# Kernel tuning notes

Hardware: AMD Instinct MI355X
Metric: run time of the kernel (lower is better)

The kernel has to match this reference:

```python
import jax, jax.numpy as jnp
import numpy as np

N, D = 4096, 2048

def setup_inputs() -> dict:
    key = jax.random.key(0)
    k1, k2 = jax.random.split(key)
    Ws = jax.random.normal(k1, (N, D), dtype=jnp.float32)
    # nn.Bilinear(D, D, 1): weight [1, D, D], bias [1]
    W = jax.random.normal(k2, (1, D, D), dtype=jnp.float32) * (1.0 / np.sqrt(D))
    b = jnp.zeros((1,), dtype=jnp.float32)
    return {"Ws": Ws, "W": W, "b": b}

def reference(Ws, W, b):
    # A[i, j] = Ws[i] @ W[0] @ Ws[j] + b[0]  (bilinear score for every pair)
    t = Ws @ W[0]                 # [N, D]
    A = t @ Ws.T + b[0]           # [N, N]
    return jax.nn.softmax(A, axis=1)
```

## Files before the change

### kernel.cpp

```cpp
#include <hip/hip_runtime.h>

typedef __bf16 bf16x8 __attribute__((ext_vector_type(8)));
typedef float f32x4 __attribute__((ext_vector_type(4)));
typedef unsigned short u16;
typedef u16 u16x8 __attribute__((ext_vector_type(8)));

#define AS1 __attribute__((address_space(1)))
#define AS3 __attribute__((address_space(3)))

__device__ __forceinline__ void split2(float x, u16& h, u16& l) {
  __bf16 hb = (__bf16)x;
  float hf = (float)hb;
  __bf16 lb = (__bf16)(x - hf);
  h = __builtin_bit_cast(u16, hb);
  l = __builtin_bit_cast(u16, lb);
}

__global__ __launch_bounds__(256) void k_pack_ws(const float* __restrict__ X,
                                                 u16* __restrict__ P) {
  const int total8 = (4096 * 2048) / 8;
  for (int idx = blockIdx.x * 256 + threadIdx.x; idx < total8; idx += gridDim.x * 256) {
    int row = idx >> 8;
    int k8  = idx & 255;
    const float* src = X + ((size_t)row << 11) + (k8 << 3);
    const float4 v0 = *(const float4*)src;
    const float4 v1 = *(const float4*)(src + 4);
    float xv[8] = {v0.x, v0.y, v0.z, v0.w, v1.x, v1.y, v1.z, v1.w};
    u16x8 hv, lv;
#pragma unroll
    for (int j = 0; j < 8; ++j) { u16 h, l; split2(xv[j], h, l); hv[j] = h; lv[j] = l; }
    size_t base = ((size_t)row << 12) + (size_t)((k8 >> 2) << 6) + ((k8 & 3) << 3);
    *(u16x8*)(P + base) = hv;
    *(u16x8*)(P + base + 32) = lv;
  }
}

__global__ __launch_bounds__(256) void k_transpose_pack_w(const float* __restrict__ W,
                                                          u16* __restrict__ P) {
  __shared__ float tile[32][33];
  const int tx = threadIdx.x, ty = threadIdx.y;
  const int kbase = blockIdx.y << 5, cbase = blockIdx.x << 5;
#pragma unroll
  for (int i = 0; i < 4; ++i)
    tile[ty * 4 + i][tx] = W[((size_t)(kbase + ty * 4 + i) << 11) + cbase + tx];
  __syncthreads();
#pragma unroll
  for (int i = 0; i < 4; ++i) {
    int c = cbase + ty * 4 + i;
    float v = tile[tx][ty * 4 + i];
    u16 h, l; split2(v, h, l);
    size_t base = ((size_t)c << 12) + (size_t)(kbase << 1) + tx;
    P[base] = h;
    P[base + 32] = l;
  }
}

template <bool SPLIT_OUT>
__global__ __launch_bounds__(256, 2) void k_gemm_nt(const u16* __restrict__ Ap,
                                                    const u16* __restrict__ Bp,
                                                    float* __restrict__ Cout,
                                                    u16* __restrict__ Cpack,
                                                    const int Ncols) {
  __shared__ __align__(16) u16 lds_a[128 * 64];
  __shared__ __align__(16) u16 lds_b[128 * 64];
  const int tid = threadIdx.x;
  const int lane = tid & 63, w = tid >> 6;
  const int wr = w >> 1, wc = w & 1;
  const int row0 = blockIdx.y << 7, col0 = blockIdx.x << 7;
  const int lrow = lane & 15, kg = lane >> 4;

  f32x4 acc[4][4] = {};

  const u16* abase = Ap + ((size_t)row0 << 12);
  const u16* bbase = Bp + ((size_t)col0 << 12);

  int offAh[4], offAl[4], offBh[4], offBl[4];
#pragma unroll
  for (int m = 0; m < 4; ++m) {
    int r = wr * 64 + m * 16 + lrow;
    int sw = r & 7;
    offAh[m] = r * 64 + ((kg ^ sw) << 3);
    offAl[m] = r * 64 + (((4 + kg) ^ sw) << 3);
    int rb = wc * 64 + m * 16 + lrow;
    int swb = rb & 7;
    offBh[m] = rb * 64 + ((kg ^ swb) << 3);
    offBl[m] = rb * 64 + (((4 + kg) ^ swb) << 3);
  }

  for (int kb = 0; kb < 64; ++kb) {
    const int kofs = kb << 6;
#pragma unroll
    for (int i = 0; i < 4; ++i) {
      int s = i * 256 + tid;
      int r = s >> 3, c = s & 7;
      int cs = c ^ (r & 7);
      __builtin_amdgcn_global_load_lds(
          (const AS1 unsigned int*)(abase + ((size_t)r << 12) + kofs + (cs << 3)),
          (AS3 unsigned int*)(lds_a + ((i * 256 + w * 64) << 3)), 16, 0, 0);
    }
#pragma unroll
    for (int i = 0; i < 4; ++i) {
      int s = i * 256 + tid;
      int r = s >> 3, c = s & 7;
      int cs = c ^ (r & 7);
      __builtin_amdgcn_global_load_lds(
          (const AS1 unsigned int*)(bbase + ((size_t)r << 12) + kofs + (cs << 3)),
          (AS3 unsigned int*)(lds_b + ((i * 256 + w * 64) << 3)), 16, 0, 0);
    }
    __syncthreads();

    bf16x8 ah[4], al[4];
#pragma unroll
    for (int m = 0; m < 4; ++m) {
      ah[m] = *(const bf16x8*)&lds_a[offAh[m]];
      al[m] = *(const bf16x8*)&lds_a[offAl[m]];
    }
#pragma unroll
    for (int n = 0; n < 4; ++n) {
      bf16x8 bh = *(const bf16x8*)&lds_b[offBh[n]];
      bf16x8 bl = *(const bf16x8*)&lds_b[offBl[n]];
#pragma unroll
      for (int m = 0; m < 4; ++m) {
        acc[m][n] = __builtin_amdgcn_mfma_f32_16x16x32_bf16(ah[m], bh, acc[m][n], 0, 0, 0);
        acc[m][n] = __builtin_amdgcn_mfma_f32_16x16x32_bf16(ah[m], bl, acc[m][n], 0, 0, 0);
        acc[m][n] = __builtin_amdgcn_mfma_f32_16x16x32_bf16(al[m], bh, acc[m][n], 0, 0, 0);
      }
    }
    __syncthreads();
  }

#pragma unroll
  for (int m = 0; m < 4; ++m) {
#pragma unroll
    for (int n = 0; n < 4; ++n) {
#pragma unroll
      for (int j = 0; j < 4; ++j) {
        int gr = row0 + wr * 64 + m * 16 + kg * 4 + j;
        int gc = col0 + wc * 64 + n * 16 + lrow;
        float x = acc[m][n][j];
        if (SPLIT_OUT) {
          u16 h, l; split2(x, h, l);
          size_t base = ((size_t)gr << 12) + (size_t)((gc >> 5) << 6) + (gc & 31);
          Cpack[base] = h;
          Cpack[base + 32] = l;
        } else {
          Cout[(size_t)gr * Ncols + gc] = x;
        }
      }
    }
  }
}

__global__ __launch_bounds__(512, 2) void k_gemm256(const u16* __restrict__ Ap,
                                                    const u16* __restrict__ Bp,
                                                    float* __restrict__ Cout) {
  __shared__ __align__(16) u16 sm[4 * 16384];
  const int tid = threadIdx.x;
  const int lane = tid & 63, w = tid >> 6;
  const int wr = w >> 2, wc = w & 3;
  const int row0 = blockIdx.y << 8, col0 = blockIdx.x << 8;
  const int lrow = lane & 15, kg = lane >> 4;
  const int sw = lrow & 7;

  const u16* Abase = Ap + ((size_t)row0 << 12);
  const u16* Bbase = Bp + ((size_t)col0 << 12);

  size_t gsrc[4];
  int dsto[4];
#pragma unroll
  for (int i = 0; i < 4; ++i) {
    int s = i * 512 + tid;
    int r = s >> 3, c = s & 7;
    int cs = c ^ (r & 7);
    gsrc[i] = ((size_t)r << 12) + (cs << 3);
    dsto[i] = (i * 512 + w * 64) << 3;
  }

  const int baseAh = (wr * 128 + lrow) * 64 + ((kg ^ sw) << 3);
  const int baseAl = (wr * 128 + lrow) * 64 + (((4 | kg) ^ sw) << 3);
  const int baseBh = (wc * 64 + lrow) * 64 + ((kg ^ sw) << 3);
  const int baseBl = (wc * 64 + lrow) * 64 + (((4 | kg) ^ sw) << 3);

  f32x4 acc[8][4] = {};

  auto stage = [&](int t, u16* la, u16* lb) {
    const int kofs = t << 6;
#pragma unroll
    for (int i = 0; i < 4; ++i)
      __builtin_amdgcn_global_load_lds((const AS1 unsigned int*)(Abase + gsrc[i] + kofs),
                                       (AS3 unsigned int*)(la + dsto[i]), 16, 0, 0);
#pragma unroll
    for (int i = 0; i < 4; ++i)
      __builtin_amdgcn_global_load_lds((const AS1 unsigned int*)(Bbase + gsrc[i] + kofs),
                                       (AS3 unsigned int*)(lb + dsto[i]), 16, 0, 0);
  };

  stage(0, sm, sm + 16384);
  stage(1, sm + 32768, sm + 49152);
  asm volatile("s_waitcnt vmcnt(8)" ::: "memory");
  __builtin_amdgcn_sched_barrier(0);
  __builtin_amdgcn_s_barrier();

  for (int t = 0; t < 64; ++t) {
    u16* la = sm + (t & 1) * 32768;
    u16* lb = la + 16384;
    bf16x8 bh[4], bl[4];
#pragma unroll
    for (int p = 0; p < 4; ++p) {
      if (p == 0) {
#pragma unroll
        for (int n = 0; n < 4; ++n) {
          bh[n] = *(const bf16x8*)&lb[baseBh + n * 1024];
          bl[n] = *(const bf16x8*)&lb[baseBl + n * 1024];
        }
      }
      bf16x8 ah0 = *(const bf16x8*)&la[baseAh + (2 * p) * 1024];
      bf16x8 al0 = *(const bf16x8*)&la[baseAl + (2 * p) * 1024];
      bf16x8 ah1 = *(const bf16x8*)&la[baseAh + (2 * p + 1) * 1024];
      bf16x8 al1 = *(const bf16x8*)&la[baseAl + (2 * p + 1) * 1024];
      __builtin_amdgcn_s_setprio(1);
#pragma unroll
      for (int n = 0; n < 4; ++n) {
        acc[2 * p][n]     = __builtin_amdgcn_mfma_f32_16x16x32_bf16(ah0, bh[n], acc[2 * p][n], 0, 0, 0);
        acc[2 * p + 1][n] = __builtin_amdgcn_mfma_f32_16x16x32_bf16(ah1, bh[n], acc[2 * p + 1][n], 0, 0, 0);
      }
#pragma unroll
      for (int n = 0; n < 4; ++n) {
        acc[2 * p][n]     = __builtin_amdgcn_mfma_f32_16x16x32_bf16(ah0, bl[n], acc[2 * p][n], 0, 0, 0);
        acc[2 * p + 1][n] = __builtin_amdgcn_mfma_f32_16x16x32_bf16(ah1, bl[n], acc[2 * p + 1][n], 0, 0, 0);
      }
#pragma unroll
      for (int n = 0; n < 4; ++n) {
        acc[2 * p][n]     = __builtin_amdgcn_mfma_f32_16x16x32_bf16(al0, bh[n], acc[2 * p][n], 0, 0, 0);
        acc[2 * p + 1][n] = __builtin_amdgcn_mfma_f32_16x16x32_bf16(al1, bh[n], acc[2 * p + 1][n], 0, 0, 0);
      }
      __builtin_amdgcn_s_setprio(0);
      if (p < 3) __builtin_amdgcn_s_barrier();
    }
    asm volatile("s_waitcnt lgkmcnt(0)" ::: "memory");
    __builtin_amdgcn_sched_barrier(0);
    __builtin_amdgcn_s_barrier();
    if (t + 2 < 64) {
      stage(t + 2, la, lb);
      asm volatile("s_waitcnt vmcnt(8)" ::: "memory");
    } else {
      asm volatile("s_waitcnt vmcnt(0)" ::: "memory");
    }
    __builtin_amdgcn_sched_barrier(0);
    __builtin_amdgcn_s_barrier();
  }

#pragma unroll
  for (int m = 0; m < 8; ++m) {
#pragma unroll
    for (int n = 0; n < 4; ++n) {
#pragma unroll
      for (int j = 0; j < 4; ++j) {
        int gr = row0 + wr * 128 + m * 16 + kg * 4 + j;
        int gc = col0 + wc * 64 + n * 16 + lrow;
        Cout[((size_t)gr << 12) + gc] = acc[m][n][j];
      }
    }
  }
}

__global__ __launch_bounds__(256) void k_softmax_rows(float* __restrict__ A) {
  const int row = blockIdx.x;
  float* p = A + ((size_t)row << 12);
  const int tid = threadIdx.x;
  const int lane = tid & 63, w = tid >> 6;
  float4 v[4];
  float mx = -3.0e38f;
#pragma unroll
  for (int i = 0; i < 4; ++i) {
    v[i] = ((const float4*)p)[tid + (i << 8)];
    mx = fmaxf(mx, fmaxf(fmaxf(v[i].x, v[i].y), fmaxf(v[i].z, v[i].w)));
  }
#pragma unroll
  for (int off = 32; off; off >>= 1) mx = fmaxf(mx, __shfl_xor(mx, off, 64));
  __shared__ float redm[4], reds[4];
  if (lane == 0) redm[w] = mx;
  __syncthreads();
  mx = fmaxf(fmaxf(redm[0], redm[1]), fmaxf(redm[2], redm[3]));
  float s = 0.f;
#pragma unroll
  for (int i = 0; i < 4; ++i) {
    v[i].x = __expf(v[i].x - mx);
    v[i].y = __expf(v[i].y - mx);
    v[i].z = __expf(v[i].z - mx);
    v[i].w = __expf(v[i].w - mx);
    s += (v[i].x + v[i].y) + (v[i].z + v[i].w);
  }
#pragma unroll
  for (int off = 32; off; off >>= 1) s += __shfl_xor(s, off, 64);
  if (lane == 0) reds[w] = s;
  __syncthreads();
  s = (reds[0] + reds[1]) + (reds[2] + reds[3]);
  const float inv = 1.0f / s;
#pragma unroll
  for (int i = 0; i < 4; ++i) {
    v[i].x *= inv; v[i].y *= inv; v[i].z *= inv; v[i].w *= inv;
    ((float4*)p)[tid + (i << 8)] = v[i];
  }
}

extern "C" void kernel_launch(void* const* d_in, const int* in_sizes, int n_in,
                              void* d_out, int out_size, void* d_ws, size_t ws_size,
                              hipStream_t stream) {
  (void)in_sizes; (void)n_in; (void)out_size; (void)ws_size;
  const float* Ws = (const float*)d_in[0];
  const float* W  = (const float*)d_in[1];
  float* out = (float*)d_out;

  u16* ws_pack = (u16*)d_ws;
  u16* wt_pack = ws_pack + (size_t)4096 * 4096;
  u16* t_pack  = wt_pack + (size_t)2048 * 4096;

  k_pack_ws<<<4096, 256, 0, stream>>>(Ws, ws_pack);
  k_transpose_pack_w<<<dim3(64, 64), dim3(32, 8), 0, stream>>>(W, wt_pack);
  k_gemm_nt<true><<<dim3(16, 32), 256, 0, stream>>>(ws_pack, wt_pack, nullptr, t_pack, 2048);
  k_gemm256<<<dim3(16, 16), 512, 0, stream>>>(t_pack, ws_pack, out);
  k_softmax_rows<<<4096, 256, 0, stream>>>(out);
}
```

Before: 278.6 us.

## Interleave per-phase global-to-LDS loads into the MFMA loop of the 256-tile GEMM

Replaces the whole-tile double-buffer staging, which issued a full stage after each k-step between two barriers, with fine-grained loads. The loop is unrolled over two k-tiles, and each of the eight compute phases issues a pair of 64-row chunk loads. Each chunk goes into a buffer region that the current phase is not reading. The goal is to spread memory traffic evenly across the MFMA work and remove the separate bulk-load synchronisation step at each tile boundary. The price is a barrier every phase and more complex buffer-hazard reasoning. The tail also issues redundant wrapped loads that are never used.

```diff
diff --git a/kernel.cpp b/kernel.cpp
--- a/kernel.cpp
+++ b/kernel.cpp
@@ -154,7 +154,7 @@
 __global__ __launch_bounds__(512, 2) void k_gemm256(const u16* __restrict__ Ap,
                                                     const u16* __restrict__ Bp,
                                                     float* __restrict__ Cout) {
-  __shared__ __align__(16) u16 sm[4 * 16384];
+  __shared__ __align__(16) u16 sm[65536];
   const int tid = threadIdx.x;
   const int lane = tid & 63, w = tid >> 6;
   const int wr = w >> 2, wc = w & 3;
@@ -165,90 +165,94 @@
   const u16* Abase = Ap + ((size_t)row0 << 12);
   const u16* Bbase = Bp + ((size_t)col0 << 12);
 
-  size_t gsrc[4];
-  int dsto[4];
-#pragma unroll
-  for (int i = 0; i < 4; ++i) {
-    int s = i * 512 + tid;
-    int r = s >> 3, c = s & 7;
-    int cs = c ^ (r & 7);
-    gsrc[i] = ((size_t)r << 12) + (cs << 3);
-    dsto[i] = (i * 512 + w * 64) << 3;
-  }
-
-  const int baseAh = (wr * 128 + lrow) * 64 + ((kg ^ sw) << 3);
-  const int baseAl = (wr * 128 + lrow) * 64 + (((4 | kg) ^ sw) << 3);
+  const size_t gsrc0 = ((size_t)(tid >> 3) << 12) + ((size_t)((tid & 7) ^ ((tid >> 3) & 7)) << 3);
+  const int dst0 = (w * 64) << 3;
+
+  auto stA = [&](int T, int j) {
+    __builtin_amdgcn_global_load_lds(
+        (const AS1 unsigned int*)(Abase + gsrc0 + ((size_t)(j * 64) << 12) + ((T & 63) << 6)),
+        (AS3 unsigned int*)(sm + ((T & 1) << 14) + j * 4096 + dst0), 16, 0, 0);
+  };
+  auto stB = [&](int T, int j) {
+    __builtin_amdgcn_global_load_lds(
+        (const AS1 unsigned int*)(Bbase + gsrc0 + ((size_t)(j * 64) << 12) + ((T & 63) << 6)),
+        (AS3 unsigned int*)(sm + 32768 + ((T & 1) << 14) + j * 4096 + dst0), 16, 0, 0);
+  };
+
+  const int baseAh = wr * 8192 + lrow * 64 + ((kg ^ sw) << 3);
+  const int baseAl = wr * 8192 + lrow * 64 + (((4 | kg) ^ sw) << 3);
   const int baseBh = (wc * 64 + lrow) * 64 + ((kg ^ sw) << 3);
   const int baseBl = (wc * 64 + lrow) * 64 + (((4 | kg) ^ sw) << 3);
 
   f32x4 acc[8][4] = {};
-
-  auto stage = [&](int t, u16* la, u16* lb) {
-    const int kofs = t << 6;
-#pragma unroll
-    for (int i = 0; i < 4; ++i)
-      __builtin_amdgcn_global_load_lds((const AS1 unsigned int*)(Abase + gsrc[i] + kofs),
-                                       (AS3 unsigned int*)(la + dsto[i]), 16, 0, 0);
-#pragma unroll
-    for (int i = 0; i < 4; ++i)
-      __builtin_amdgcn_global_load_lds((const AS1 unsigned int*)(Bbase + gsrc[i] + kofs),
-                                       (AS3 unsigned int*)(lb + dsto[i]), 16, 0, 0);
-  };
-
-  stage(0, sm, sm + 16384);
-  stage(1, sm + 32768, sm + 49152);
-  asm volatile("s_waitcnt vmcnt(8)" ::: "memory");
+  bf16x8 bh[4], bl[4];
+
+  stA(0, 0); stA(0, 1); stA(0, 2); stA(0, 3);
+  stB(0, 0); stB(0, 1); stB(0, 2); stB(0, 3);
+  stB(1, 0); stB(1, 1); stB(1, 2); stB(1, 3);
+  stA(1, 0); stA(1, 2);
+  asm volatile("s_waitcnt vmcnt(6)" ::: "memory");
   __builtin_amdgcn_sched_barrier(0);
   __builtin_amdgcn_s_barrier();
 
-  for (int t = 0; t < 64; ++t) {
-    u16* la = sm + (t & 1) * 32768;
-    u16* lb = la + 16384;
-    bf16x8 bh[4], bl[4];
-#pragma unroll
-    for (int p = 0; p < 4; ++p) {
-      if (p == 0) {
+  for (int i = 0; i < 32; ++i) {
+    const int t0 = 2 * i;
+#pragma unroll
+    for (int p = 0; p < 8; ++p) {
+      const int q = p & 3;
+      const int t = t0 + (p >> 2);
+      const u16* la = sm + ((t & 1) << 14);
+      const u16* lb = sm + 32768 + ((t & 1) << 14);
+      if (q == 0) {
 #pragma unroll
         for (int n = 0; n < 4; ++n) {
           bh[n] = *(const bf16x8*)&lb[baseBh + n * 1024];
           bl[n] = *(const bf16x8*)&lb[baseBl + n * 1024];
         }
       }
-      bf16x8 ah0 = *(const bf16x8*)&la[baseAh + (2 * p) * 1024];
-      bf16x8 al0 = *(const bf16x8*)&la[baseAl + (2 * p) * 1024];
-      bf16x8 ah1 = *(const bf16x8*)&la[baseAh + (2 * p + 1) * 1024];
-      bf16x8 al1 = *(const bf16x8*)&la[baseAl + (2 * p + 1) * 1024];
+      bf16x8 ah0 = *(const bf16x8*)&la[baseAh + (2 * q) * 1024];
+      bf16x8 al0 = *(const bf16x8*)&la[baseAl + (2 * q) * 1024];
+      bf16x8 ah1 = *(const bf16x8*)&la[baseAh + (2 * q + 1) * 1024];
+      bf16x8 al1 = *(const bf16x8*)&la[baseAl + (2 * q + 1) * 1024];
+      switch (p) {
+        case 0: stA(t0 + 1, 1); stA(t0 + 1, 3); break;
+        case 1: stB(t0 + 2, 0); stB(t0 + 2, 1); break;
+        case 2: stB(t0 + 2, 2); stB(t0 + 2, 3); break;
+        case 3: stA(t0 + 2, 0); stA(t0 + 2, 2); break;
+        case 4: stA(t0 + 2, 1); stA(t0 + 2, 3); break;
+        case 5: stB(t0 + 3, 0); stB(t0 + 3, 1); break;
+        case 6: stB(t0 + 3, 2); stB(t0 + 3, 3); break;
+        case 7: stA(t0 + 3, 0); stA(t0 + 3, 2); break;
+      }
+      __builtin_amdgcn_s_barrier();
       __builtin_amdgcn_s_setprio(1);
+      const int m0 = 2 * q, m1 = 2 * q + 1;
 #pragma unroll
       for (int n = 0; n < 4; ++n) {
-        acc[2 * p][n]     = __builtin_amdgcn_mfma_f32_16x16x32_bf16(ah0, bh[n], acc[2 * p][n], 0, 0, 0);
-        acc[2 * p + 1][n] = __builtin_amdgcn_mfma_f32_16x16x32_bf16(ah1, bh[n], acc[2 * p + 1][n], 0, 0, 0);
+        acc[m0][n] = __builtin_amdgcn_mfma_f32_16x16x32_bf16(ah0, bh[n], acc[m0][n], 0, 0, 0);
+        acc[m1][n] = __builtin_amdgcn_mfma_f32_16x16x32_bf16(ah1, bh[n], acc[m1][n], 0, 0, 0);
       }
 #pragma unroll
       for (int n = 0; n < 4; ++n) {
-        acc[2 * p][n]     = __builtin_amdgcn_mfma_f32_16x16x32_bf16(ah0, bl[n], acc[2 * p][n], 0, 0, 0);
-        acc[2 * p + 1][n] = __builtin_amdgcn_mfma_f32_16x16x32_bf16(ah1, bl[n], acc[2 * p + 1][n], 0, 0, 0);
+        acc[m0][n] = __builtin_amdgcn_mfma_f32_16x16x32_bf16(ah0, bl[n], acc[m0][n], 0, 0, 0);
+        acc[m1][n] = __builtin_amdgcn_mfma_f32_16x16x32_bf16(ah1, bl[n], acc[m1][n], 0, 0, 0);
       }
 #pragma unroll
       for (int n = 0; n < 4; ++n) {
-        acc[2 * p][n]     = __builtin_amdgcn_mfma_f32_16x16x32_bf16(al0, bh[n], acc[2 * p][n], 0, 0, 0);
-        acc[2 * p + 1][n] = __builtin_amdgcn_mfma_f32_16x16x32_bf16(al1, bh[n], acc[2 * p + 1][n], 0, 0, 0);
+        acc[m0][n] = __builtin_amdgcn_mfma_f32_16x16x32_bf16(al0, bh[n], acc[m0][n], 0, 0, 0);
+        acc[m1][n] = __builtin_amdgcn_mfma_f32_16x16x32_bf16(al1, bh[n], acc[m1][n], 0, 0, 0);
       }
       __builtin_amdgcn_s_setprio(0);
-      if (p < 3) __builtin_amdgcn_s_barrier();
-    }
-    asm volatile("s_waitcnt lgkmcnt(0)" ::: "memory");
-    __builtin_amdgcn_sched_barrier(0);
-    __builtin_amdgcn_s_barrier();
-    if (t + 2 < 64) {
-      stage(t + 2, la, lb);
-      asm volatile("s_waitcnt vmcnt(8)" ::: "memory");
-    } else {
-      asm volatile("s_waitcnt vmcnt(0)" ::: "memory");
-    }
-    __builtin_amdgcn_sched_barrier(0);
-    __builtin_amdgcn_s_barrier();
-  }
+      asm volatile("s_waitcnt lgkmcnt(0)" ::: "memory");
+      __builtin_amdgcn_sched_barrier(0);
+      if (q == 3) {
+        asm volatile("s_waitcnt vmcnt(6)" ::: "memory");
+        __builtin_amdgcn_sched_barrier(0);
+      }
+      __builtin_amdgcn_s_barrier();
+    }
+  }
+  asm volatile("s_waitcnt vmcnt(0)" ::: "memory");
 
 #pragma unroll
   for (int m = 0; m < 8; ++m) {
```

Measured after the change: 263.6 us. -5.4%, faster.
